# Performance work log

Hardware: AMD Instinct MI355X
Metric: run time of the kernel (lower is better)

## Reference

```python
import jax, jax.numpy as jnp
import numpy as np

B, S, DQ, DK, H, D = 4, 2048, 1024, 1024, 16, 64


def setup_inputs() -> dict:
    key = jax.random.key(0)
    k1, k2, k3, k4 = jax.random.split(key, 4)
    # xavier_uniform bound for Linear(in, out): sqrt(6/(in+out))
    bq = float(np.sqrt(6.0 / (DQ + H * D)))
    bk = float(np.sqrt(6.0 / (DK + H * D)))
    return {
        "query_input": jax.random.normal(k1, (B, S, DQ), dtype=jnp.float32),
        "key_input": jax.random.normal(k2, (B, S, DK), dtype=jnp.float32),
        "Wq": jax.random.uniform(k3, (H * D, DQ), minval=-bq, maxval=bq, dtype=jnp.float32),
        "bq": jnp.zeros((H * D,), dtype=jnp.float32),
        "Wk": jax.random.uniform(k4, (H * D, DK), minval=-bk, maxval=bk, dtype=jnp.float32),
        "bk": jnp.zeros((H * D,), dtype=jnp.float32),
    }


def reference(query_input, key_input, Wq, bq, Wk, bk):
    scaling = D ** (-0.5)
    # projections: (B, S, H*D) -> (B, S, H, D)
    q = (query_input @ Wq.T + bq).reshape(B, S, H, D) * scaling
    k = (key_input @ Wk.T + bk).reshape(B, S, H, D)
    # scores: (B, H, S, S), softmax over keys
    scores = jnp.einsum("bqhd,bkhd->bhqk", q, k)
    attn = jax.nn.softmax(scores, axis=-1)
    # NOTE: module reuses K as the value tensor (no V projection)
    out = jnp.einsum("bhqk,bkhd->bqhd", attn, k)
    return out.reshape(B, S, H * D)
```

## Files before the change

kernel.cpp:

```cpp
#include <hip/hip_runtime.h>
#include <stdint.h>

#define NB 4
#define NS 2048
#define NH 16
#define ND 64
#define NHD 1024
#define NK 1024

typedef __attribute__((ext_vector_type(8))) short short8;
typedef __attribute__((ext_vector_type(4))) float f32x4;
typedef __attribute__((ext_vector_type(16))) float f32x16;
typedef __attribute__((ext_vector_type(4))) unsigned u32x4;

__device__ __forceinline__ unsigned short f2bf(float f) {
    union { float f; unsigned u; } v; v.f = f;
    return (unsigned short)((v.u + 0x7fffu + ((v.u >> 16) & 1u)) >> 16);
}

__device__ __forceinline__ void gload_lds16(const unsigned short* g, unsigned short* l) {
    __builtin_amdgcn_global_load_lds(
        (const __attribute__((address_space(1))) void*)g,
        (__attribute__((address_space(3))) void*)l, 16, 0, 0);
}

__device__ __forceinline__ unsigned cvtpk(float lo, float hi) {
    unsigned r;
    asm volatile("v_cvt_pk_bf16_f32 %0, %1, %2" : "=v"(r) : "v"(lo), "v"(hi));
    return r;
}
__device__ __forceinline__ void plswap(unsigned& a, unsigned& b) {
    asm volatile("v_permlane32_swap_b32 %0, %1" : "+v"(a), "+v"(b));
}
__device__ __forceinline__ float exp2_raw(float x) {
    float r;
    asm("v_exp_f32 %0, %1" : "=v"(r) : "v"(x));
    return r;
}

__global__ void cvt_w_bf16(const float* __restrict__ Wq, const float* __restrict__ Wk,
                           unsigned short* __restrict__ Wqb, unsigned short* __restrict__ Wkb) {
    const int n4 = (NK * NHD) / 4;
    const int stride = gridDim.x * blockDim.x;
    for (int i = blockIdx.x * blockDim.x + threadIdx.x; i < 2 * n4; i += stride) {
        const int m = i < n4 ? 0 : 1;
        const int j = m ? i - n4 : i;
        const float4 v = m ? ((const float4*)Wk)[j] : ((const float4*)Wq)[j];
        ushort4 o;
        o.x = f2bf(v.x); o.y = f2bf(v.y); o.z = f2bf(v.z); o.w = f2bf(v.w);
        if (m) ((ushort4*)Wkb)[j] = o; else ((ushort4*)Wqb)[j] = o;
    }
}

__global__ __launch_bounds__(256) void proj_gemm2(
    const float* __restrict__ Xq,
    const float* __restrict__ Xk,
    const unsigned short* __restrict__ Wqb,
    const unsigned short* __restrict__ Wkb,
    const float* __restrict__ bqv,
    const float* __restrict__ bkv,
    unsigned short* __restrict__ Qo,
    unsigned short* __restrict__ Ko,
    unsigned short* __restrict__ KTo,
    float qscale)
{
    const int Bid = blockIdx.x;
    const int xcd = Bid & 7;
    const int j = Bid >> 3;
    const int nb = j & 7;
    const int p = xcd * 16 + (j >> 3);
    const int which = p >> 6;
    const int mb = p & 63;

    const float* A32           = which ? Xk : Xq;
    const unsigned short* Wt   = which ? Wkb : Wqb;
    const float* bias          = which ? bkv : bqv;
    unsigned short* outp       = which ? Ko : Qo;
    unsigned short* outT       = which ? KTo : nullptr;
    const float scale          = which ? 1.0f : qscale;

    __shared__ __attribute__((aligned(16))) unsigned short Ah[128 * 64];
    __shared__ __attribute__((aligned(16))) unsigned short Bh[2][128 * 64];
    const int t = threadIdx.x;
    const int lane = t & 63;
    const int w = t >> 6;
    const int wm = (w >> 1) * 64, wn = (w & 1) * 64;
    const int lr = lane & 15, lg = lane >> 4;
    const long bm = (long)mb * 128;
    const long bn = (long)nb * 128;

    f32x4 acc[4][4];
    #pragma unroll
    for (int i = 0; i < 4; ++i)
        #pragma unroll
        for (int jj = 0; jj < 4; ++jj) acc[i][jj] = (f32x4){0.f, 0.f, 0.f, 0.f};

    auto LOADA = [&](float4 (&a)[8], int k0) {
        #pragma unroll
        for (int c = 0; c < 4; ++c) {
            const int u2 = c * 256 + t;
            const int row = u2 >> 3, c8 = u2 & 7;
            const float* src = A32 + (bm + row) * (long)NK + k0 + c8 * 8;
            a[2 * c]     = *(const float4*)src;
            a[2 * c + 1] = *(const float4*)(src + 4);
        }
    };
    auto WRITEA = [&](float4 (&a)[8]) {
        char* Ab = (char*)Ah;
        #pragma unroll
        for (int c = 0; c < 4; ++c) {
            const int u2 = c * 256 + t;
            const int row = u2 >> 3;
            const int cbyte = ((u2 & 7) << 4) ^ ((row & 7) << 4);
            u32x4 wv;
            wv[0] = cvtpk(a[2 * c].x, a[2 * c].y);
            wv[1] = cvtpk(a[2 * c].z, a[2 * c].w);
            wv[2] = cvtpk(a[2 * c + 1].x, a[2 * c + 1].y);
            wv[3] = cvtpk(a[2 * c + 1].z, a[2 * c + 1].w);
            *(u32x4*)(Ab + (row << 7) + cbyte) = wv;
        }
    };
    const int scolB = (((lane & 7) ^ (lane >> 3)) << 3);
    auto BGLOAD = [&](int k0, int buf) {
        #pragma unroll
        for (int c = 0; c < 4; ++c) {
            const int rowB = c * 32 + w * 8 + (lane >> 3);
            gload_lds16(Wt + (bn + rowB) * NK + k0 + scolB,
                        &Bh[buf][(size_t)(c * 256 + w * 64) * 8]);
        }
    };

    auto KSTEP = [&](int it, float4 (&a)[8]) {
        asm volatile("s_waitcnt lgkmcnt(0)" ::: "memory");
        __builtin_amdgcn_s_barrier();
        __builtin_amdgcn_sched_barrier(0);
        WRITEA(a);
        if (it + 1 < 16) BGLOAD((it + 1) * 64, (it + 1) & 1);
        if (it + 2 < 16) LOADA(a, (it + 2) * 64);
        if (it < 14) asm volatile("s_waitcnt vmcnt(20)" ::: "memory");
        else         asm volatile("s_waitcnt vmcnt(0)" ::: "memory");
        asm volatile("s_waitcnt lgkmcnt(0)" ::: "memory");
        __builtin_amdgcn_s_barrier();
        __builtin_amdgcn_sched_barrier(0);

        const char* Ab = (const char*)Ah;
        const char* Bb = (const char*)Bh[it & 1];
        #pragma unroll
        for (int kk = 0; kk < 2; ++kk) {
            short8 af[4], bfr[4];
            const int swzr = (lr & 7) << 4;
            #pragma unroll
            for (int mi = 0; mi < 4; ++mi) {
                const int rowA = wm + mi * 16 + lr;
                af[mi] = *(const short8*)(Ab + (rowA << 7) + ((kk * 64 + lg * 16) ^ swzr));
            }
            #pragma unroll
            for (int ni = 0; ni < 4; ++ni) {
                const int rowB = wn + ni * 16 + lr;
                bfr[ni] = *(const short8*)(Bb + (rowB << 7) + ((kk * 64 + lg * 16) ^ swzr));
            }
            #pragma unroll
            for (int mi = 0; mi < 4; ++mi)
                #pragma unroll
                for (int ni = 0; ni < 4; ++ni)
                    acc[mi][ni] = __builtin_amdgcn_mfma_f32_16x16x32_bf16(af[mi], bfr[ni], acc[mi][ni], 0, 0, 0);
        }
    };

    float4 aA[8], aB[8];
    BGLOAD(0, 0);
    LOADA(aA, 0);
    LOADA(aB, 64);
    for (int it2 = 0; it2 < 8; ++it2) {
        KSTEP(2 * it2, aA);
        KSTEP(2 * it2 + 1, aB);
    }

    #pragma unroll
    for (int ni = 0; ni < 4; ++ni) {
        const int n = (int)bn + wn + ni * 16 + lr;
        const float bv = bias[n];
        const int h = n >> 6, d = n & 63;
        #pragma unroll
        for (int mi = 0; mi < 4; ++mi) {
            const int m0 = (int)bm + wm + mi * 16 + lg * 4;
            const int b = m0 >> 11, s0 = m0 & 2047;
            unsigned short vv[4];
            #pragma unroll
            for (int r = 0; r < 4; ++r) {
                const float v = (acc[mi][ni][r] + bv) * scale;
                vv[r] = f2bf(v);
                outp[(((size_t)(b * NH + h)) * NS + (s0 + r)) * ND + d] = vv[r];
            }
            if (outT) {
                ushort4 tv; tv.x = vv[0]; tv.y = vv[1]; tv.z = vv[2]; tv.w = vv[3];
                *(ushort4*)&outT[(((size_t)(b * NH + h)) * ND + d) * NS + s0] = tv;
            }
        }
    }
}

#define PACK_P(s0, s1, paw, lsum)                                              \
    do {                                                                       \
        _Pragma("unroll")                                                      \
        for (int tt_ = 0; tt_ < 2; ++tt_) {                                    \
            unsigned c_[8];                                                    \
            _Pragma("unroll")                                                  \
            for (int j_ = 0; j_ < 8; ++j_) {                                   \
                const float plo_ = exp2_raw(tt_ ? s1[2 * j_]     : s0[2 * j_]);   \
                const float phi_ = exp2_raw(tt_ ? s1[2 * j_ + 1] : s0[2 * j_ + 1]); \
                (lsum) += plo_ + phi_;                                         \
                c_[j_] = cvtpk(plo_, phi_);                                    \
            }                                                                  \
            plswap(c_[0], c_[2]); plswap(c_[1], c_[3]);                        \
            plswap(c_[4], c_[6]); plswap(c_[5], c_[7]);                        \
            paw[2 * tt_]     = (u32x4){c_[0], c_[1], c_[2], c_[3]};            \
            paw[2 * tt_ + 1] = (u32x4){c_[4], c_[5], c_[6], c_[7]};            \
        }                                                                      \
    } while (0)

__global__ __launch_bounds__(512, 4) void attn_fused(
    const unsigned short* __restrict__ Qb,
    const unsigned short* __restrict__ Kb,
    const unsigned short* __restrict__ KTb,
    float* __restrict__ outp)
{
    __shared__ __attribute__((aligned(16))) unsigned short LDSA[2 * 2 * 4096];

    const int t = threadIdx.x;
    const int lane = t & 63;
    const int wq = t >> 6;
    const int q5 = lane & 31;
    const int hi = lane >> 5;

    const int Bid = blockIdx.x + 8 * blockIdx.y + 128 * blockIdx.z;
    const int xcd = Bid & 7;
    const int wIdx = Bid >> 3;
    const int qblk = wIdx & 7;
    const int g = xcd * 8 + (wIdx >> 3);
    const int h = g & 15, b = g >> 4;
    const int qbase = qblk * 256 + wq * 32;

    const unsigned short* Qh  = Qb  + ((size_t)(b * NH + h)) * NS * ND;
    const unsigned short* Kh  = Kb  + ((size_t)(b * NH + h)) * NS * ND;
    const unsigned short* KTh = KTb + ((size_t)(b * NH + h)) * ND * NS;

    short8 qB[4];
    {
        const unsigned short* Qrow = Qh + (size_t)(qbase + q5) * ND;
        #pragma unroll
        for (int kd = 0; kd < 4; ++kd)
            qB[kd] = *(const short8*)&Qrow[kd * 16 + hi * 8];
    }

    const int srow = wq * 8 + (lane >> 3);
    const int scol = ((((lane & 7) << 4) ^ ((srow & 7) << 4)) >> 1);

    f32x16 acc0, acc1;
    float l_run = 0.f;
    #pragma unroll
    for (int r = 0; r < 16; ++r) { acc0[r] = 0.f; acc1[r] = 0.f; }

    auto STAGE = [&](int buf, int kti) {
        unsigned short* Kd  = &LDSA[buf * 8192];
        unsigned short* Ktd = Kd + 4096;
        const int kt = kti * 64;
        gload_lds16(Kh  + (size_t)(kt + srow) * ND + scol, Kd  + wq * 512);
        gload_lds16(KTh + (size_t)srow * NS + kt + scol,   Ktd + wq * 512);
    };

    STAGE(0, 0);
    for (int kti = 0; kti < NS / 64; ++kti) {
        const int cur = kti & 1;
        asm volatile("s_waitcnt vmcnt(0)" ::: "memory");
        __syncthreads();
        if (kti < NS / 64 - 1) STAGE(cur ^ 1, kti + 1);

        const char* Kbuf  = (const char*)&LDSA[cur * 8192];
        const char* Ktbuf = Kbuf + 8192;
        const int swz = (q5 & 7) << 4;
        const int ro0 = q5 * 128, ro1 = ro0 + 4096;

        f32x16 s0, s1;
        #pragma unroll
        for (int r = 0; r < 16; ++r) { s0[r] = 0.f; s1[r] = 0.f; }
        __builtin_amdgcn_s_setprio(1);
        #pragma unroll
        for (int kd = 0; kd < 4; ++kd) {
            const int cb = (kd * 32 + hi * 16) ^ swz;
            short8 kf0 = *(const short8*)(Kbuf + ro0 + cb);
            short8 kf1 = *(const short8*)(Kbuf + ro1 + cb);
            s0 = __builtin_amdgcn_mfma_f32_32x32x16_bf16(kf0, qB[kd], s0, 0, 0, 0);
            s1 = __builtin_amdgcn_mfma_f32_32x32x16_bf16(kf1, qB[kd], s1, 0, 0, 0);
        }
        __builtin_amdgcn_s_setprio(0);

        u32x4 paw[4];
        PACK_P(s0, s1, paw, l_run);

        __builtin_amdgcn_s_setprio(1);
        #pragma unroll
        for (int ks = 0; ks < 4; ++ks) {
            union { u32x4 u; short8 s; } pa; pa.u = paw[ks];
            const int cb = (ks * 32 + hi * 16) ^ swz;
            short8 vf0 = *(const short8*)(Ktbuf + ro0 + cb);
            short8 vf1 = *(const short8*)(Ktbuf + ro1 + cb);
            acc0 = __builtin_amdgcn_mfma_f32_32x32x16_bf16(pa.s, vf0, acc0, 0, 0, 0);
            acc1 = __builtin_amdgcn_mfma_f32_32x32x16_bf16(pa.s, vf1, acc1, 0, 0, 0);
        }
        __builtin_amdgcn_s_setprio(0);
    }

    const float lt = l_run + __shfl_xor(l_run, 32);
    const float inv = 1.0f / lt;
    #pragma unroll
    for (int r = 0; r < 16; ++r) {
        const int qr = (r & 3) + 8 * (r >> 2) + 4 * hi;
        const float invr = __shfl(inv, qr);
        float* orow = outp + ((size_t)b * NS + (qbase + qr)) * NHD + h * ND;
        orow[q5]      = acc0[r] * invr;
        orow[32 + q5] = acc1[r] * invr;
    }
}

extern "C" void kernel_launch(void* const* d_in, const int* in_sizes, int n_in,
                              void* d_out, int out_size, void* d_ws, size_t ws_size,
                              hipStream_t stream) {
    const float* xq = (const float*)d_in[0];
    const float* xk = (const float*)d_in[1];
    const float* Wq = (const float*)d_in[2];
    const float* bq = (const float*)d_in[3];
    const float* Wk = (const float*)d_in[4];
    const float* bk = (const float*)d_in[5];
    float* outp = (float*)d_out;

    unsigned short* Wqb = (unsigned short*)d_ws;
    unsigned short* Wkb = Wqb + 1048576;
    unsigned short* Qb  = Wkb + 1048576;
    unsigned short* Kb  = Qb  + 8388608;
    unsigned short* KTb = Kb  + 8388608;

    cvt_w_bf16<<<1024, 256, 0, stream>>>(Wq, Wk, Wqb, Wkb);

    const float qscale = 0.125f * 1.4426950408889634f;
    proj_gemm2<<<1024, 256, 0, stream>>>(xq, xk, Wqb, Wkb, bq, bk,
                                         Qb, Kb, KTb, qscale);

    attn_fused<<<dim3(8, 16, 4), 512, 0, stream>>>(Qb, Kb, KTb, outp);
}
```

Baseline: 142.6 us.

## Restructure projection GEMM into 256x256 tiles with phased ping-pong pipeline

Replaces the 128x128-tile projection GEMM (1024 blocks of 256 threads) with a 256x256-tile version using 512 threads, double-buffered A and B in 128KB of dynamic LDS. The k-loop is split into four phases that interleave LDS fragment reads, the next tile's global loads and LDS writes, and MFMA groups under raised wave priority. The intent is more operand reuse per load and better overlap of memory traffic with matrix math. In exchange, the grid is only 256 blocks, the large LDS footprint limits occupancy, and the extra barriers per phase add synchronisation cost.

Result: no change. 141.9 us (-0.5%).

```diff
diff --git a/kernel.cpp b/kernel.cpp
--- a/kernel.cpp
+++ b/kernel.cpp
@@ -52,7 +52,35 @@
     }
 }
 
-__global__ __launch_bounds__(256) void proj_gemm2(
+#define PH_SYNC() do { __builtin_amdgcn_s_barrier(); __builtin_amdgcn_sched_barrier(0); \
+    asm volatile("s_waitcnt lgkmcnt(0)" ::: "memory"); __builtin_amdgcn_sched_barrier(0); } while (0)
+#define PH_END()  do { __builtin_amdgcn_s_barrier(); __builtin_amdgcn_sched_barrier(0); } while (0)
+
+#define RD_AF(MH, KK)                                                                     \
+    _Pragma("unroll")                                                                     \
+    for (int mi_ = 0; mi_ < 4; ++mi_) {                                                   \
+        const int rowA_ = wm + (MH) * 64 + mi_ * 16 + lr;                                 \
+        af[mi_] = *(const short8*)(Ab + (rowA_ << 7) + (((KK) * 64 + lg * 16) ^ swzr));   \
+    }
+#define RD_BF(KK)                                                                         \
+    _Pragma("unroll")                                                                     \
+    for (int ni_ = 0; ni_ < 4; ++ni_) {                                                   \
+        const int rowB_ = wn + ni_ * 16 + lr;                                             \
+        bfr[ni_] = *(const short8*)(Bb + (rowB_ << 7) + (((KK) * 64 + lg * 16) ^ swzr));  \
+    }
+#define DO_MFMA(MH)                                                                       \
+    do {                                                                                  \
+        __builtin_amdgcn_s_setprio(1);                                                    \
+        _Pragma("unroll")                                                                 \
+        for (int mi_ = 0; mi_ < 4; ++mi_)                                                 \
+            _Pragma("unroll")                                                             \
+            for (int ni_ = 0; ni_ < 4; ++ni_)                                             \
+                acc[(MH) * 4 + mi_][ni_] = __builtin_amdgcn_mfma_f32_16x16x32_bf16(       \
+                    af[mi_], bfr[ni_], acc[(MH) * 4 + mi_][ni_], 0, 0, 0);                \
+        __builtin_amdgcn_s_setprio(0);                                                    \
+    } while (0)
+
+__global__ __launch_bounds__(512, 2) void proj_gemm3(
     const float* __restrict__ Xq,
     const float* __restrict__ Xk,
     const unsigned short* __restrict__ Wqb,
@@ -64,116 +92,107 @@
     unsigned short* __restrict__ KTo,
     float qscale)
 {
-    const int Bid = blockIdx.x;
-    const int xcd = Bid & 7;
-    const int j = Bid >> 3;
-    const int nb = j & 7;
-    const int p = xcd * 16 + (j >> 3);
-    const int which = p >> 6;
-    const int mb = p & 63;
-
-    const float* A32           = which ? Xk : Xq;
-    const unsigned short* Wt   = which ? Wkb : Wqb;
-    const float* bias          = which ? bkv : bqv;
-    unsigned short* outp       = which ? Ko : Qo;
-    unsigned short* outT       = which ? KTo : nullptr;
-    const float scale          = which ? 1.0f : qscale;
-
-    __shared__ __attribute__((aligned(16))) unsigned short Ah[128 * 64];
-    __shared__ __attribute__((aligned(16))) unsigned short Bh[2][128 * 64];
+    extern __shared__ __attribute__((aligned(16))) char smem[];
+
+    const int bid = blockIdx.x;
+    const int wg = (bid & 7) * 32 + (bid >> 3);
+    const int mp = wg >> 2;
+    const int nb = wg & 3;
+    const int which = mp >> 5;
+    const long bm = (long)(mp & 31) * 256;
+    const long bn = (long)nb * 256;
+
+    const float* A32         = which ? Xk : Xq;
+    const unsigned short* Wt = which ? Wkb : Wqb;
+    const float* bias        = which ? bkv : bqv;
+    unsigned short* outp     = which ? Ko : Qo;
+    unsigned short* outT     = which ? KTo : nullptr;
+    const float scale        = which ? 1.0f : qscale;
+
     const int t = threadIdx.x;
     const int lane = t & 63;
     const int w = t >> 6;
-    const int wm = (w >> 1) * 64, wn = (w & 1) * 64;
+    const int wm = (w >> 2) * 128, wn = (w & 3) * 64;
     const int lr = lane & 15, lg = lane >> 4;
-    const long bm = (long)mb * 128;
-    const long bn = (long)nb * 128;
-
-    f32x4 acc[4][4];
+    const int swzr = (lr & 7) << 4;
+
+    f32x4 acc[8][4];
     #pragma unroll
-    for (int i = 0; i < 4; ++i)
+    for (int i = 0; i < 8; ++i)
         #pragma unroll
         for (int jj = 0; jj < 4; ++jj) acc[i][jj] = (f32x4){0.f, 0.f, 0.f, 0.f};
 
-    auto LOADA = [&](float4 (&a)[8], int k0) {
+    float4 aset[8];
+
+    auto LOADA = [&](int k0) {
         #pragma unroll
         for (int c = 0; c < 4; ++c) {
-            const int u2 = c * 256 + t;
+            const int u2 = c * 512 + t;
             const int row = u2 >> 3, c8 = u2 & 7;
             const float* src = A32 + (bm + row) * (long)NK + k0 + c8 * 8;
-            a[2 * c]     = *(const float4*)src;
-            a[2 * c + 1] = *(const float4*)(src + 4);
+            aset[2 * c]     = *(const float4*)src;
+            aset[2 * c + 1] = *(const float4*)(src + 4);
         }
     };
-    auto WRITEA = [&](float4 (&a)[8]) {
-        char* Ab = (char*)Ah;
+    auto WRITEA = [&](int buf) {
+        char* Ad = smem + buf * 32768;
         #pragma unroll
         for (int c = 0; c < 4; ++c) {
-            const int u2 = c * 256 + t;
+            const int u2 = c * 512 + t;
             const int row = u2 >> 3;
             const int cbyte = ((u2 & 7) << 4) ^ ((row & 7) << 4);
             u32x4 wv;
-            wv[0] = cvtpk(a[2 * c].x, a[2 * c].y);
-            wv[1] = cvtpk(a[2 * c].z, a[2 * c].w);
-            wv[2] = cvtpk(a[2 * c + 1].x, a[2 * c + 1].y);
-            wv[3] = cvtpk(a[2 * c + 1].z, a[2 * c + 1].w);
-            *(u32x4*)(Ab + (row << 7) + cbyte) = wv;
+            wv[0] = cvtpk(aset[2 * c].x, aset[2 * c].y);
+            wv[1] = cvtpk(aset[2 * c].z, aset[2 * c].w);
+            wv[2] = cvtpk(aset[2 * c + 1].x, aset[2 * c + 1].y);
+            wv[3] = cvtpk(aset[2 * c + 1].z, aset[2 * c + 1].w);
+            *(u32x4*)(Ad + (row << 7) + cbyte) = wv;
         }
     };
     const int scolB = (((lane & 7) ^ (lane >> 3)) << 3);
     auto BGLOAD = [&](int k0, int buf) {
+        unsigned short* Bd = (unsigned short*)(smem + 65536 + buf * 32768);
         #pragma unroll
         for (int c = 0; c < 4; ++c) {
-            const int rowB = c * 32 + w * 8 + (lane >> 3);
-            gload_lds16(Wt + (bn + rowB) * NK + k0 + scolB,
-                        &Bh[buf][(size_t)(c * 256 + w * 64) * 8]);
+            const int rowB = c * 64 + w * 8 + (lane >> 3);
+            gload_lds16(Wt + (bn + rowB) * (long)NK + k0 + scolB,
+                        Bd + (size_t)(c * 64 + w * 8) * 64);
         }
     };
 
-    auto KSTEP = [&](int it, float4 (&a)[8]) {
-        asm volatile("s_waitcnt lgkmcnt(0)" ::: "memory");
-        __builtin_amdgcn_s_barrier();
-        __builtin_amdgcn_sched_barrier(0);
-        WRITEA(a);
-        if (it + 1 < 16) BGLOAD((it + 1) * 64, (it + 1) & 1);
-        if (it + 2 < 16) LOADA(a, (it + 2) * 64);
-        if (it < 14) asm volatile("s_waitcnt vmcnt(20)" ::: "memory");
-        else         asm volatile("s_waitcnt vmcnt(0)" ::: "memory");
-        asm volatile("s_waitcnt lgkmcnt(0)" ::: "memory");
-        __builtin_amdgcn_s_barrier();
-        __builtin_amdgcn_sched_barrier(0);
-
-        const char* Ab = (const char*)Ah;
-        const char* Bb = (const char*)Bh[it & 1];
-        #pragma unroll
-        for (int kk = 0; kk < 2; ++kk) {
-            short8 af[4], bfr[4];
-            const int swzr = (lr & 7) << 4;
-            #pragma unroll
-            for (int mi = 0; mi < 4; ++mi) {
-                const int rowA = wm + mi * 16 + lr;
-                af[mi] = *(const short8*)(Ab + (rowA << 7) + ((kk * 64 + lg * 16) ^ swzr));
-            }
-            #pragma unroll
-            for (int ni = 0; ni < 4; ++ni) {
-                const int rowB = wn + ni * 16 + lr;
-                bfr[ni] = *(const short8*)(Bb + (rowB << 7) + ((kk * 64 + lg * 16) ^ swzr));
-            }
-            #pragma unroll
-            for (int mi = 0; mi < 4; ++mi)
-                #pragma unroll
-                for (int ni = 0; ni < 4; ++ni)
-                    acc[mi][ni] = __builtin_amdgcn_mfma_f32_16x16x32_bf16(af[mi], bfr[ni], acc[mi][ni], 0, 0, 0);
-        }
-    };
-
-    float4 aA[8], aB[8];
     BGLOAD(0, 0);
-    LOADA(aA, 0);
-    LOADA(aB, 64);
-    for (int it2 = 0; it2 < 8; ++it2) {
-        KSTEP(2 * it2, aA);
-        KSTEP(2 * it2 + 1, aB);
+    asm volatile("" ::: "memory");
+    LOADA(0);
+    asm volatile("" ::: "memory");
+    WRITEA(0);
+    __builtin_amdgcn_sched_barrier(0);
+    LOADA(64);
+    asm volatile("s_waitcnt lgkmcnt(0)" ::: "memory");
+    __builtin_amdgcn_s_barrier();
+    __builtin_amdgcn_sched_barrier(0);
+
+    for (int it = 0; it < 16; ++it) {
+        const int cur = it & 1;
+        const char* Ab = (const char*)smem + cur * 32768;
+        const char* Bb = (const char*)smem + 65536 + cur * 32768;
+        short8 af[4], bfr[4];
+
+        RD_BF(0); RD_AF(0, 0);
+        if (it + 1 < 16) BGLOAD((it + 1) * 64, cur ^ 1);
+        PH_SYNC(); DO_MFMA(0); PH_END();
+
+        RD_AF(1, 0);
+        if (it + 1 < 16) WRITEA(cur ^ 1);
+        PH_SYNC(); DO_MFMA(1); PH_END();
+
+        RD_BF(1); RD_AF(0, 1);
+        if (it + 2 < 16) LOADA((it + 2) * 64);
+        PH_SYNC(); DO_MFMA(0); PH_END();
+
+        RD_AF(1, 1);
+        if (it + 2 < 16)      asm volatile("s_waitcnt vmcnt(8)" ::: "memory");
+        else if (it + 1 < 16) asm volatile("s_waitcnt vmcnt(0)" ::: "memory");
+        PH_SYNC(); DO_MFMA(1); PH_END();
     }
 
     #pragma unroll
@@ -182,7 +201,7 @@
         const float bv = bias[n];
         const int h = n >> 6, d = n & 63;
         #pragma unroll
-        for (int mi = 0; mi < 4; ++mi) {
+        for (int mi = 0; mi < 8; ++mi) {
             const int m0 = (int)bm + wm + mi * 16 + lg * 4;
             const int b = m0 >> 11, s0 = m0 & 2047;
             unsigned short vv[4];
@@ -340,11 +359,18 @@
     unsigned short* Kb  = Qb  + 8388608;
     unsigned short* KTb = Kb  + 8388608;
 
+    static bool lds_init = false;
+    if (!lds_init) {
+        hipFuncSetAttribute((const void*)proj_gemm3,
+                            hipFuncAttributeMaxDynamicSharedMemorySize, 131072);
+        lds_init = true;
+    }
+
     cvt_w_bf16<<<1024, 256, 0, stream>>>(Wq, Wk, Wqb, Wkb);
 
     const float qscale = 0.125f * 1.4426950408889634f;
-    proj_gemm2<<<1024, 256, 0, stream>>>(xq, xk, Wqb, Wkb, bq, bk,
-                                         Qb, Kb, KTb, qscale);
+    proj_gemm3<<<256, 512, 131072, stream>>>(xq, xk, Wqb, Wkb, bq, bk,
+                                             Qb, Kb, KTb, qscale);
 
     attn_fused<<<dim3(8, 16, 4), 512, 0, stream>>>(Qb, Kb, KTb, outp);
 }
```
